# Kernel optimization log

Measured on AMD Instinct MI355X. Metric: run time of the kernel, lower is better.

## Reference

```python
import jax, jax.numpy as jnp
import numpy as np

B, S, D, H = 4, 2048, 128, 8

def setup_inputs() -> dict:
    key = jax.random.key(0)
    ks = jax.random.split(key, 11)
    sc_in = 1.0 / np.sqrt(D)
    sc_out = 1.0 / np.sqrt(H * D)
    return {
        "Q": jax.random.normal(ks[0], (B, S, D), jnp.float32),
        "K": jax.random.normal(ks[1], (B, S, D), jnp.float32),
        "V": jax.random.normal(ks[2], (B, S, D), jnp.float32),
        "WQ_w": jax.random.normal(ks[3], (H * D, D), jnp.float32) * sc_in,
        "WQ_b": jax.random.normal(ks[4], (H * D,), jnp.float32) * 0.01,
        "WK_w": jax.random.normal(ks[5], (H * D, D), jnp.float32) * sc_in,
        "WK_b": jax.random.normal(ks[6], (H * D,), jnp.float32) * 0.01,
        "WV_w": jax.random.normal(ks[7], (H * D, D), jnp.float32) * sc_in,
        "WV_b": jax.random.normal(ks[8], (H * D,), jnp.float32) * 0.01,
        "W_w": jax.random.normal(ks[9], (D, H * D), jnp.float32) * sc_out,
        "W_b": jax.random.normal(ks[10], (D,), jnp.float32) * 0.01,
    }

def reference(Q, K, V, WQ_w, WQ_b, WK_w, WK_b, WV_w, WV_b, W_w, W_b):
    b, s, d = Q.shape
    h = WQ_w.shape[0] // d
    # Linear projections: [b,s,d] -> [b,s,h*d] -> [b,h,s,d]
    rQ = (Q @ WQ_w.T + WQ_b).reshape(b, s, h, d).transpose(0, 2, 1, 3)
    rK = (K @ WK_w.T + WK_b).reshape(b, s, h, d).transpose(0, 2, 1, 3)
    rV = (V @ WV_w.T + WV_b).reshape(b, s, h, d).transpose(0, 2, 1, 3)
    # Scores: [b,h,s,s], scaled by sqrt(head_dim) = sqrt(input_dim)
    scores = jnp.einsum("bhqd,bhkd->bhqk", rQ, rK) / jnp.sqrt(jnp.asarray(d, rQ.dtype))
    sim = jax.nn.softmax(scores, axis=-1)
    # Attend and merge heads: [b,h,s,d] -> [b,s,h*d]
    oV = jnp.einsum("bhqk,bhkd->bqhd", sim, rV).reshape(b, s, h * d)
    return oV @ W_w.T + W_b
```

## Files before the change

kernel.cpp:

```cpp
#include <hip/hip_runtime.h>
#include <hip/hip_bf16.h>

typedef unsigned short u16;
typedef unsigned int   u32;
typedef short v8s __attribute__((ext_vector_type(8)));
typedef float v4f __attribute__((ext_vector_type(4)));
typedef float v16f __attribute__((ext_vector_type(16)));

#define MFMA16(a,b,c) __builtin_amdgcn_mfma_f32_16x16x32_bf16(a,b,c,0,0,0)
#define MFMA32(a,b,c) __builtin_amdgcn_mfma_f32_32x32x16_bf16(a,b,c,0,0,0)


__device__ __forceinline__ float b2f(u16 u){ u32 i = ((u32)u)<<16; float f; __builtin_memcpy(&f,&i,4); return f; }
__device__ __forceinline__ u16 f2b(float f){ u32 i; __builtin_memcpy(&i,&f,4); u32 r = (i + 0x7FFFu + ((i>>16)&1u))>>16; return (u16)r; }
__device__ __forceinline__ u32 pk2(float a, float b){
  __hip_bfloat162 h = __float22bfloat162_rn(make_float2(a,b));
  u32 r; __builtin_memcpy(&r,&h,4); return r;
}

__device__ __forceinline__ void gl16(const void* g, void* l){
  __builtin_amdgcn_global_load_lds((const __attribute__((address_space(1))) u32*)g,
                                   (__attribute__((address_space(3))) u32*)l, 16, 0, 0);
}

__device__ __forceinline__ void stage8f(const float* g, u16* l){
  float4 a = *(const float4*)g, b = *(const float4*)(g+4);
  union { u16 h[8]; uint4 q; } u;
  u.h[0]=f2b(a.x); u.h[1]=f2b(a.y); u.h[2]=f2b(a.z); u.h[3]=f2b(a.w);
  u.h[4]=f2b(b.x); u.h[5]=f2b(b.y); u.h[6]=f2b(b.z); u.h[7]=f2b(b.w);
  *(uint4*)l = u.q;
}

__global__ __launch_bounds__(256) void proj_qkv(
    const float* __restrict__ Qx, const float* __restrict__ Kx, const float* __restrict__ Vx,
    const float* __restrict__ WQw, const float* __restrict__ WQb,
    const float* __restrict__ WKw, const float* __restrict__ WKb,
    const float* __restrict__ WVw, const float* __restrict__ WVb,
    u16* __restrict__ Qp, u16* __restrict__ Kp, u16* __restrict__ Vt)
{
  __shared__ u16 smem[32768];
  u16* As = smem;
  u16* Ws = smem + 16384;

  const int z = blockIdx.z;
  const float* X    = (z==0) ? Qx  : (z==1 ? Kx  : Vx);
  const float* W    = (z==0) ? WQw : (z==1 ? WKw : WVw);
  const float* bias = (z==0) ? WQb : (z==1 ? WKb : WVb);
  u16* out          = (z==0) ? Qp  : (z==1 ? Kp  : Vt);

  const int tid = threadIdx.x, wv = tid>>6, lane = tid&63;
  const int quad = lane>>4, l16 = lane&15;
  const int r4 = lane>>2, c4 = lane&3;
  const int m0 = blockIdx.x*128, n0 = blockIdx.y*128;

  for (int idx = wv; idx < 32; idx += 4) {
    int kt = idx >> 3, rg = idx & 7;
    int row = rg*16 + r4;
    stage8f(X + (size_t)(m0+row)*128 + kt*32 + c4*8, &As[kt*4096 + rg*512 + lane*8]);
    stage8f(W + (size_t)(n0+row)*128 + kt*32 + c4*8, &Ws[kt*4096 + rg*512 + lane*8]);
  }
  __syncthreads();

  const int wm = wv & 1, wn = wv >> 1;
  v4f acc[4][4];
#pragma unroll
  for (int i=0;i<4;i++)
#pragma unroll
    for (int j=0;j<4;j++) acc[i][j] = (v4f){0.f,0.f,0.f,0.f};

  if (z < 2) {
#pragma unroll
    for (int ks=0; ks<4; ++ks) {
      v8s af[4], bf[4];
#pragma unroll
      for (int mi=0; mi<4; ++mi) af[mi] = *(const v8s*)&As[ks*4096 + (wm*64+mi*16+l16)*32 + quad*8];
#pragma unroll
      for (int ni=0; ni<4; ++ni) bf[ni] = *(const v8s*)&Ws[ks*4096 + (wn*64+ni*16+l16)*32 + quad*8];
#pragma unroll
      for (int mi=0; mi<4; ++mi)
#pragma unroll
        for (int ni=0; ni<4; ++ni)
          acc[mi][ni] = MFMA16(bf[ni], af[mi], acc[mi][ni]);
    }
#pragma unroll
    for (int ni=0; ni<4; ++ni) {
      int nb = n0 + wn*64 + ni*16 + quad*4;
      float bv0 = bias[nb+0];
      float bv1 = bias[nb+1];
      float bv2 = bias[nb+2];
      float bv3 = bias[nb+3];
      int h = n0 >> 7, dh = nb & 127;
#pragma unroll
      for (int mi=0; mi<4; ++mi) {
        int m = m0 + wm*64 + mi*16 + l16;
        int b = m >> 11, s = m & 2047;
        uint2 pk;
        pk.x = (u32)f2b(acc[mi][ni][0] + bv0) | ((u32)f2b(acc[mi][ni][1] + bv1) << 16);
        pk.y = (u32)f2b(acc[mi][ni][2] + bv2) | ((u32)f2b(acc[mi][ni][3] + bv3) << 16);
        *(uint2*)&out[(size_t)(((b<<3) + h)*2048 + s)*128 + dh] = pk;
      }
    }
  } else {
#pragma unroll
    for (int ks=0; ks<4; ++ks) {
      v8s af[4], bf[4];
#pragma unroll
      for (int mi=0; mi<4; ++mi) af[mi] = *(const v8s*)&As[ks*4096 + (wm*64+mi*16+l16)*32 + quad*8];
#pragma unroll
      for (int ni=0; ni<4; ++ni) bf[ni] = *(const v8s*)&Ws[ks*4096 + (wn*64+ni*16+l16)*32 + quad*8];
#pragma unroll
      for (int mi=0; mi<4; ++mi)
#pragma unroll
        for (int ni=0; ni<4; ++ni)
          acc[mi][ni] = MFMA16(af[mi], bf[ni], acc[mi][ni]);
    }
    __syncthreads();
    u16* Cs = smem;
#pragma unroll
    for (int ni=0; ni<4; ++ni) {
      int nl = wn*64 + ni*16 + l16;
      float bv = bias[n0 + nl];
#pragma unroll
      for (int mi=0; mi<4; ++mi) {
        int ml = wm*64 + mi*16 + quad*4;
        uint2 pk;
        pk.x = (u32)f2b(acc[mi][ni][0] + bv) | ((u32)f2b(acc[mi][ni][1] + bv) << 16);
        pk.y = (u32)f2b(acc[mi][ni][2] + bv) | ((u32)f2b(acc[mi][ni][3] + bv) << 16);
        *(uint2*)&Cs[nl*136 + ml] = pk;
      }
    }
    __syncthreads();
    const int nl = tid >> 1;
    const int mb = (tid & 1) * 64;
    const int h = (n0 + nl) >> 7, dh = (n0 + nl) & 127;
    const int b = m0 >> 11, s0 = m0 & 2047;
    size_t gbase = (((size_t)((b<<3) + h)*128 + dh)*2048) + s0 + mb;
    size_t lbase = (size_t)nl*136 + mb;
#pragma unroll
    for (int j = 0; j < 8; ++j)
      *(uint4*)&out[gbase + j*8] = *(const uint4*)&Cs[lbase + j*8];
  }
}

__global__ __launch_bounds__(256, 2) void attn(
    const u16* __restrict__ Qp, const u16* __restrict__ Kp,
    const u16* __restrict__ Vt, u16* __restrict__ O)
{
  __shared__ u16 smem[32768];

  const int tid = threadIdx.x, wv = tid>>6, lane = tid&63;
  const int l32 = lane&31, h = lane>>5;

  const int n  = blockIdx.x;
  const int bh = (n&7)*4 + (n>>7);
  const int q0 = ((n>>3)&15) * 128;

  const u16* Qb = Qp + (size_t)bh*262144 + (size_t)q0*128;
  const u16* Kb = Kp + (size_t)bh*262144;
  const u16* Vb = Vt + (size_t)bh*262144;

  for (int r = 0; r < 8; ++r) {
    int idx = r*256 + tid;
    int kd = idx>>8, q = (idx>>1)&127, hh = idx&1;
    gl16(Qb + q*128 + kd*16 + hh*8, &smem[idx*8]);
  }
  __syncthreads();
  const int qrow = wv*32 + l32;
  v8s qf[8];
#pragma unroll
  for (int kd = 0; kd < 8; ++kd)
    qf[kd] = *(const v8s*)&smem[kd*2048 + qrow*16 + h*8];
  __syncthreads();

  int gK[4], gV[4], lK[4], lV[4];
#pragma unroll
  for (int r = 0; r < 4; ++r) {
    int idx = r*256 + tid;
    int kd = idx>>7, key = (idx>>1)&63, hh = idx&1;
    gK[r] = key*128 + kd*16 + hh*8;  lK[r] = idx*8;
    int kt = idx>>8, d = (idx>>1)&127;
    gV[r] = d*2048 + kt*16 + hh*8;   lV[r] = 16384 + idx*8;
  }

  v8s onesf;
#pragma unroll
  for (int j = 0; j < 8; ++j) onesf[j] = (short)0x3F80;

  v16f oacc[4], lacc;
#pragma unroll
  for (int nt = 0; nt < 4; ++nt)
#pragma unroll
    for (int j = 0; j < 16; ++j) oacc[nt][j] = 0.f;
#pragma unroll
  for (int j = 0; j < 16; ++j) lacc[j] = 0.f;

  const float C2 = 0.12751743076f;
  const float CB = -64.0f * C2;

#pragma unroll
  for (int r = 0; r < 4; ++r) gl16(Kb + gK[r], &smem[lK[r]]);
#pragma unroll
  for (int r = 0; r < 4; ++r) gl16(Vb + gV[r], &smem[lV[r]]);

  for (int it = 0; it < 32; ++it) {
    const int cur = it & 1;
    const int ko = cur*8192;
    const int vo = cur*8192;
    __syncthreads();

    if (it + 1 < 32) {
      const u16* Kt  = Kb + (it+1)*8192;
      const u16* Vtt = Vb + (it+1)*64;
      const int po = (cur^1)*8192;
#pragma unroll
      for (int r = 0; r < 4; ++r) gl16(Kt  + gK[r], &smem[po + lK[r]]);
#pragma unroll
      for (int r = 0; r < 4; ++r) gl16(Vtt + gV[r], &smem[po + lV[r]]);
    }

    v16f sa[2];
#pragma unroll
    for (int m = 0; m < 2; ++m)
#pragma unroll
      for (int j = 0; j < 16; ++j) sa[m][j] = 0.f;
#pragma unroll
    for (int kd = 0; kd < 8; ++kd) {
#pragma unroll
      for (int m = 0; m < 2; ++m) {
        v8s kf = *(const v8s*)&smem[ko + kd*1024 + (m*32 + l32)*16 + h*8];
        sa[m] = MFMA32(kf, qf[kd], sa[m]);
      }
    }

    u32 P32[2][4][2];
#pragma unroll
    for (int m = 0; m < 2; ++m)
#pragma unroll
      for (int g = 0; g < 4; ++g) {
        P32[m][g][0] = pk2(exp2f(fmaf(sa[m][g*4+0], C2, CB)),
                           exp2f(fmaf(sa[m][g*4+1], C2, CB)));
        P32[m][g][1] = pk2(exp2f(fmaf(sa[m][g*4+2], C2, CB)),
                           exp2f(fmaf(sa[m][g*4+3], C2, CB)));
      }

    v8s pf[4];
#pragma unroll
    for (int kt = 0; kt < 4; ++kt) {
      const int m = kt >> 1, e = (kt & 1) * 2, o = e + 1;
      u32 t0 = h ? P32[m][e][0] : P32[m][o][0];
      u32 t1 = h ? P32[m][e][1] : P32[m][o][1];
      u32 r0 = (u32)__shfl_xor((int)t0, 32);
      u32 r1 = (u32)__shfl_xor((int)t1, 32);
      union { u32 u[4]; v8s s; } f;
      f.u[0] = h ? r0 : P32[m][e][0];
      f.u[1] = h ? r1 : P32[m][e][1];
      f.u[2] = h ? P32[m][o][0] : r0;
      f.u[3] = h ? P32[m][o][1] : r1;
      pf[kt] = f.s;
    }

#pragma unroll
    for (int kt = 0; kt < 4; ++kt) {
      lacc = MFMA32(pf[kt], onesf, lacc);
#pragma unroll
      for (int nt = 0; nt < 4; ++nt) {
        v8s vf = *(const v8s*)&smem[16384 + vo + kt*2048 + (nt*32 + l32)*16 + h*8];
        oacc[nt] = MFMA32(pf[kt], vf, oacc[nt]);
      }
    }
  }

  const int b = bh >> 3, hd = bh & 7;
#pragma unroll
  for (int reg = 0; reg < 16; ++reg) {
    int q = q0 + wv*32 + (reg&3) + 8*(reg>>2) + 4*h;
    float inv = 1.0f / lacc[reg];
    size_t base = ((size_t)(b*2048 + q))*1024 + hd*128;
#pragma unroll
    for (int nt = 0; nt < 4; ++nt)
      O[base + nt*32 + l32] = f2b(oacc[nt][reg] * inv);
  }
}

__global__ __launch_bounds__(256) void outproj(
    const u16* __restrict__ A, const float* __restrict__ Ww,
    const float* __restrict__ Wb, float* __restrict__ out)
{
  __shared__ u16 As[2048];
  __shared__ u16 Ws[8192];

  const int tid = threadIdx.x, wv = tid>>6, lane = tid&63;
  const int quad = lane>>4, l16 = lane&15;
  const int r4 = lane>>2, c4 = lane&3;
  const int m0 = blockIdx.x*32;

  v4f acc[2][2];
#pragma unroll
  for (int i=0;i<2;i++)
#pragma unroll
    for (int j=0;j<2;j++) acc[i][j] = (v4f){0.f,0.f,0.f,0.f};

  for (int kb = 0; kb < 1024; kb += 64) {
    {
      int kt = wv >> 1, rg = wv & 1;
      int row = rg*16 + r4;
      gl16(A + (size_t)(m0+row)*1024 + kb + kt*32 + c4*8, &As[kt*1024 + rg*512 + lane*8]);
    }
    for (int idx = wv; idx < 16; idx += 4) {
      int kt = idx >> 3, rg = idx & 7;
      int row = rg*16 + r4;
      stage8f(Ww + (size_t)row*1024 + kb + kt*32 + c4*8, &Ws[kt*4096 + rg*512 + lane*8]);
    }
    __syncthreads();
#pragma unroll
    for (int ks = 0; ks < 2; ++ks) {
      v8s af0 = *(const v8s*)&As[ks*1024 + (l16)*32 + quad*8];
      v8s af1 = *(const v8s*)&As[ks*1024 + (16 + l16)*32 + quad*8];
#pragma unroll
      for (int nj = 0; nj < 2; ++nj) {
        v8s bf = *(const v8s*)&Ws[ks*4096 + ((wv*2+nj)*16 + l16)*32 + quad*8];
        acc[0][nj] = MFMA16(af0, bf, acc[0][nj]);
        acc[1][nj] = MFMA16(af1, bf, acc[1][nj]);
      }
    }
    __syncthreads();
  }

#pragma unroll
  for (int nj = 0; nj < 2; ++nj) {
    int col = (wv*2+nj)*16 + l16;
    float bv = Wb[col];
#pragma unroll
    for (int mi = 0; mi < 2; ++mi) {
#pragma unroll
      for (int r = 0; r < 4; ++r) {
        int row = m0 + mi*16 + quad*4 + r;
        out[(size_t)row*128 + col] = acc[mi][nj][r] + bv;
      }
    }
  }
}

extern "C" void kernel_launch(void* const* d_in, const int* in_sizes, int n_in,
                              void* d_out, int out_size, void* d_ws, size_t ws_size,
                              hipStream_t stream) {
  const float* Q   = (const float*)d_in[0];
  const float* K   = (const float*)d_in[1];
  const float* V   = (const float*)d_in[2];
  const float* WQw = (const float*)d_in[3];
  const float* WQb = (const float*)d_in[4];
  const float* WKw = (const float*)d_in[5];
  const float* WKb = (const float*)d_in[6];
  const float* WVw = (const float*)d_in[7];
  const float* WVb = (const float*)d_in[8];
  const float* Ww  = (const float*)d_in[9];
  const float* Wb  = (const float*)d_in[10];
  u16* ws = (u16*)d_ws;

  const size_t SZ = (size_t)4*8*2048*128;
  u16* Qp = ws;
  u16* Kp = Qp + SZ;
  u16* Vt = Kp + SZ;
  u16* Ow = Vt + SZ;

  hipLaunchKernelGGL(proj_qkv, dim3(64,8,3), dim3(256), 0, stream,
                     Q,K,V,WQw,WQb,WKw,WKb,WVw,WVb,Qp,Kp,Vt);
  hipLaunchKernelGGL(attn, dim3(512), dim3(256), 0, stream, Qp,Kp,Vt,Ow);
  hipLaunchKernelGGL(outproj, dim3(256), dim3(256), 0, stream, Ow, Ww, Wb, (float*)d_out);
}
```

Baseline: 227.2 us.

## Split attention work across waves by head-dim halves with 64-query tiles

Each attention block now covers 64 queries instead of 128, and the grid doubles to 1024 blocks. The four waves are split into two query groups times two head-dim halves, so each wave holds half the output accumulators. K is now single-buffered while V stays double-buffered, which cuts shared memory and raises the occupancy target to 3 blocks per CU. The cost is that each pair of waves computes the QK scores twice, an extra barrier per iteration, and the row sums passing through shared memory.

```diff
diff --git a/kernel.cpp b/kernel.cpp
--- a/kernel.cpp
+++ b/kernel.cpp
@@ -142,53 +142,57 @@
   }
 }
 
-__global__ __launch_bounds__(256, 2) void attn(
+__global__ __launch_bounds__(256, 3) void attn(
     const u16* __restrict__ Qp, const u16* __restrict__ Kp,
     const u16* __restrict__ Vt, u16* __restrict__ O)
 {
-  __shared__ u16 smem[32768];
+  __shared__ u16 smem[24576];
 
   const int tid = threadIdx.x, wv = tid>>6, lane = tid&63;
   const int l32 = lane&31, h = lane>>5;
+  const int qg = wv & 1;
+  const int dh = wv >> 1;
 
   const int n  = blockIdx.x;
-  const int bh = (n&7)*4 + (n>>7);
-  const int q0 = ((n>>3)&15) * 128;
+  const int bh = (n&7)*4 + (n>>8);
+  const int q0 = ((n>>3)&31) * 64;
 
   const u16* Qb = Qp + (size_t)bh*262144 + (size_t)q0*128;
   const u16* Kb = Kp + (size_t)bh*262144;
   const u16* Vb = Vt + (size_t)bh*262144;
 
-  for (int r = 0; r < 8; ++r) {
-    int idx = r*256 + tid;
-    int kd = idx>>8, q = (idx>>1)&127, hh = idx&1;
-    gl16(Qb + q*128 + kd*16 + hh*8, &smem[idx*8]);
-  }
-  __syncthreads();
-  const int qrow = wv*32 + l32;
-  v8s qf[8];
-#pragma unroll
-  for (int kd = 0; kd < 8; ++kd)
-    qf[kd] = *(const v8s*)&smem[kd*2048 + qrow*16 + h*8];
-  __syncthreads();
-
-  int gK[4], gV[4], lK[4], lV[4];
 #pragma unroll
   for (int r = 0; r < 4; ++r) {
     int idx = r*256 + tid;
+    int kd = idx>>7, q = (idx>>1)&63, hh = idx&1;
+    gl16(Qb + q*128 + kd*16 + hh*8, &smem[idx*8]);
+  }
+  __syncthreads();
+  const int qrow = qg*32 + l32;
+  v8s qf[8];
+#pragma unroll
+  for (int kd = 0; kd < 8; ++kd)
+    qf[kd] = *(const v8s*)&smem[kd*1024 + qrow*16 + h*8];
+  __syncthreads();
+
+  int gK[4], gV[4], lKV[4];
+#pragma unroll
+  for (int r = 0; r < 4; ++r) {
+    int idx = r*256 + tid;
+    lKV[r] = idx*8;
     int kd = idx>>7, key = (idx>>1)&63, hh = idx&1;
-    gK[r] = key*128 + kd*16 + hh*8;  lK[r] = idx*8;
+    gK[r] = key*128 + kd*16 + hh*8;
     int kt = idx>>8, d = (idx>>1)&127;
-    gV[r] = d*2048 + kt*16 + hh*8;   lV[r] = 16384 + idx*8;
+    gV[r] = d*2048 + kt*16 + hh*8;
   }
 
   v8s onesf;
 #pragma unroll
   for (int j = 0; j < 8; ++j) onesf[j] = (short)0x3F80;
 
-  v16f oacc[4], lacc;
-#pragma unroll
-  for (int nt = 0; nt < 4; ++nt)
+  v16f oacc[2], lacc;
+#pragma unroll
+  for (int nt = 0; nt < 2; ++nt)
 #pragma unroll
     for (int j = 0; j < 16; ++j) oacc[nt][j] = 0.f;
 #pragma unroll
@@ -198,38 +202,35 @@
   const float CB = -64.0f * C2;
 
 #pragma unroll
-  for (int r = 0; r < 4; ++r) gl16(Kb + gK[r], &smem[lK[r]]);
-#pragma unroll
-  for (int r = 0; r < 4; ++r) gl16(Vb + gV[r], &smem[lV[r]]);
+  for (int r = 0; r < 4; ++r) gl16(Kb + gK[r], &smem[lKV[r]]);
+#pragma unroll
+  for (int r = 0; r < 4; ++r) gl16(Vb + gV[r], &smem[8192 + lKV[r]]);
+  __syncthreads();
 
   for (int it = 0; it < 32; ++it) {
-    const int cur = it & 1;
-    const int ko = cur*8192;
-    const int vo = cur*8192;
+    v16f sa[2];
+#pragma unroll
+    for (int m = 0; m < 2; ++m)
+#pragma unroll
+      for (int j = 0; j < 16; ++j) sa[m][j] = 0.f;
+#pragma unroll
+    for (int kd = 0; kd < 8; ++kd) {
+#pragma unroll
+      for (int m = 0; m < 2; ++m) {
+        v8s kf = *(const v8s*)&smem[kd*1024 + (m*32 + l32)*16 + h*8];
+        sa[m] = MFMA32(kf, qf[kd], sa[m]);
+      }
+    }
     __syncthreads();
 
     if (it + 1 < 32) {
       const u16* Kt  = Kb + (it+1)*8192;
       const u16* Vtt = Vb + (it+1)*64;
-      const int po = (cur^1)*8192;
-#pragma unroll
-      for (int r = 0; r < 4; ++r) gl16(Kt  + gK[r], &smem[po + lK[r]]);
-#pragma unroll
-      for (int r = 0; r < 4; ++r) gl16(Vtt + gV[r], &smem[po + lV[r]]);
-    }
-
-    v16f sa[2];
-#pragma unroll
-    for (int m = 0; m < 2; ++m)
-#pragma unroll
-      for (int j = 0; j < 16; ++j) sa[m][j] = 0.f;
-#pragma unroll
-    for (int kd = 0; kd < 8; ++kd) {
-#pragma unroll
-      for (int m = 0; m < 2; ++m) {
-        v8s kf = *(const v8s*)&smem[ko + kd*1024 + (m*32 + l32)*16 + h*8];
-        sa[m] = MFMA32(kf, qf[kd], sa[m]);
-      }
+      const int vpo = 8192 + ((it+1)&1)*8192;
+#pragma unroll
+      for (int r = 0; r < 4; ++r) gl16(Kt  + gK[r], &smem[lKV[r]]);
+#pragma unroll
+      for (int r = 0; r < 4; ++r) gl16(Vtt + gV[r], &smem[vpo + lKV[r]]);
     }
 
     u32 P32[2][4][2];
@@ -259,25 +260,36 @@
       pf[kt] = f.s;
     }
 
+    const int vbase = 8192 + (it&1)*8192;
 #pragma unroll
     for (int kt = 0; kt < 4; ++kt) {
-      lacc = MFMA32(pf[kt], onesf, lacc);
-#pragma unroll
-      for (int nt = 0; nt < 4; ++nt) {
-        v8s vf = *(const v8s*)&smem[16384 + vo + kt*2048 + (nt*32 + l32)*16 + h*8];
+      if (dh == 0) lacc = MFMA32(pf[kt], onesf, lacc);
+#pragma unroll
+      for (int nt = 0; nt < 2; ++nt) {
+        int d = dh*64 + nt*32 + l32;
+        v8s vf = *(const v8s*)&smem[vbase + kt*2048 + d*16 + h*8];
         oacc[nt] = MFMA32(pf[kt], vf, oacc[nt]);
       }
     }
-  }
+    __syncthreads();
+  }
+
+  float* lsh = (float*)smem;
+  if (dh == 0) {
+#pragma unroll
+    for (int reg = 0; reg < 16; ++reg)
+      lsh[qg*1024 + reg*64 + lane] = lacc[reg];
+  }
+  __syncthreads();
 
   const int b = bh >> 3, hd = bh & 7;
 #pragma unroll
   for (int reg = 0; reg < 16; ++reg) {
-    int q = q0 + wv*32 + (reg&3) + 8*(reg>>2) + 4*h;
-    float inv = 1.0f / lacc[reg];
-    size_t base = ((size_t)(b*2048 + q))*1024 + hd*128;
-#pragma unroll
-    for (int nt = 0; nt < 4; ++nt)
+    int q = q0 + qg*32 + (reg&3) + 8*(reg>>2) + 4*h;
+    float inv = 1.0f / lsh[qg*1024 + reg*64 + lane];
+    size_t base = ((size_t)(b*2048 + q))*1024 + hd*128 + dh*64;
+#pragma unroll
+    for (int nt = 0; nt < 2; ++nt)
       O[base + nt*32 + l32] = f2b(oacc[nt][reg] * inv);
   }
 }
@@ -365,6 +377,6 @@
 
   hipLaunchKernelGGL(proj_qkv, dim3(64,8,3), dim3(256), 0, stream,
                      Q,K,V,WQw,WQb,WKw,WKb,WVw,WVb,Qp,Kp,Vt);
-  hipLaunchKernelGGL(attn, dim3(512), dim3(256), 0, stream, Qp,Kp,Vt,Ow);
+  hipLaunchKernelGGL(attn, dim3(1024), dim3(256), 0, stream, Qp,Kp,Vt,Ow);
   hipLaunchKernelGGL(outproj, dim3(256), dim3(256), 0, stream, Ow, Ww, Wb, (float*)d_out);
 }
```

New measurement: 289.0 us. 27.2% more time.
